# Optimization experiments

Measured on AMD Instinct MI355X. Metric: run time of the kernel, lower is better.

Reference implementation:

```python
import jax, jax.numpy as jnp
import numpy as np

T, B, S = 50, 64, 100
H, C = 512, 512
V_TGT, V_EXT = 32000, 5000
UNK = 0  # ext_dict.stoi[UNK_WORD]


def setup_inputs() -> dict:
    key = jax.random.key(0)
    ks = jax.random.split(key, 8)
    return {
        "hidden": jax.random.normal(ks[0], (T, B, H), jnp.float32),
        "dec_rnn_output": jax.random.normal(ks[1], (T, B, H), jnp.float32),
        "concat_c": jax.random.normal(ks[2], (T, B, H + C), jnp.float32),
        "attn": jax.random.uniform(ks[3], (T, B, S), jnp.float32),
        "copy_to_ext": jax.random.randint(ks[4], (S, B), 0, V_EXT, jnp.int64),
        "W": jax.random.normal(ks[5], (V_TGT, H), jnp.float32) * 0.02,
        "b": jnp.zeros((V_TGT,), jnp.float32),
        "Wc": jax.random.normal(ks[6], (1, H), jnp.float32) * 0.02,
        "bc": jnp.zeros((1,), jnp.float32),
    }


def _safe_log(v):
    return jnp.log(jnp.clip(v, 0.001, 1.0 - 0.001))


def reference(hidden, dec_rnn_output, concat_c, attn, copy_to_ext, W, b, Wc, bc):
    # standard softmax over tgt vocab
    logits = jnp.einsum("tbh,vh->tbv", hidden, W) + b          # [T,B,V_TGT]
    prob_log = jax.nn.log_softmax(logits, axis=-1)
    # copy gate p(z) from decoder hidden (copy_prb == 'hidden')
    copy = jax.nn.sigmoid(jnp.einsum("tbh,oh->tbo", dec_rnn_output, Wc) + bc)  # [T,B,1]
    mul_attn = attn * (1.0 - copy)                              # [T,B,S]
    # onehot+bmm == masked scatter-add of attn mass into ext-vocab bins
    mask = (copy_to_ext != UNK).astype(mul_attn.dtype)          # [S,B]
    aw = mul_attn * mask.T[None]                                # [T,B,S]

    def scatter_one(a_ts, idx_s):  # a_ts [T,S], idx_s [S]
        return jnp.zeros((T, V_EXT), a_ts.dtype).at[:, idx_s].add(a_ts)

    ext_copy_prob = jax.vmap(scatter_one, in_axes=(1, 1), out_axes=1)(aw, copy_to_ext)  # [T,B,V_EXT]
    ext_copy_prob_log = _safe_log(ext_copy_prob)
    return jnp.concatenate([prob_log, ext_copy_prob_log], axis=-1)  # [T,B,V_TGT+V_EXT]
```

## Files before the change

### kernel.cpp

```cpp
#include <hip/hip_runtime.h>
#include <hip/hip_bf16.h>

#define TT 50
#define BB 64
#define SS 100
#define HH 512
#define VT 32000
#define VE 5000
#define LDC 37000
#define MROWS 3200
#define NTILE 250
#define TSTR 136

typedef __bf16 bf16x8 __attribute__((ext_vector_type(8)));
typedef float f32x4 __attribute__((ext_vector_type(4)));

__device__ __forceinline__ ushort f2bf(float f) {
    unsigned u = __float_as_uint(f);
    u += 0x7fffu + ((u >> 16) & 1u);
    return (ushort)(u >> 16);
}
__device__ __forceinline__ float bflo(unsigned u) { return __uint_as_float(u << 16); }
__device__ __forceinline__ float bfhi(unsigned u) { return __uint_as_float(u & 0xffff0000u); }

__global__ void convert_kernel(const float* __restrict__ W, const float* __restrict__ hid,
                               ushort* __restrict__ wsB, ushort* __restrict__ wsA) {
    int g = blockIdx.x * 256 + threadIdx.x;
    const int WG = 4096000;
    float4 v;
    ushort* dst;
    if (g < WG) {
        v = ((const float4*)W)[g];
        dst = wsB + 4 * (size_t)g;
    } else {
        int h = g - WG;
        v = ((const float4*)hid)[h];
        dst = wsA + 4 * (size_t)h;
    }
    ushort4 o;
    o.x = f2bf(v.x); o.y = f2bf(v.y); o.z = f2bf(v.z); o.w = f2bf(v.w);
    *(ushort4*)dst = o;
}

__global__ __launch_bounds__(256) void gemm_kernel(const ushort* __restrict__ A,
                                                   const ushort* __restrict__ B,
                                                   const float* __restrict__ bias,
                                                   ushort* __restrict__ outu,
                                                   float* __restrict__ pm,
                                                   float* __restrict__ ps) {
    __shared__ char smem[34816];
    const int tid  = threadIdx.x;
    const int w    = tid >> 6;
    const int lane = tid & 63;
    const int wr   = w >> 1, wc = w & 1;
    const int brow = blockIdx.y * 128;
    const int bcol = blockIdx.x * 128;
    const int lr   = lane & 15;
    const int kg   = lane >> 4;

    ushort* tileT = (ushort*)smem;
    const int c0 = tid, c1 = tid + 256;
    const int r0 = c0 >> 2, k0 = c0 & 3;
    const int r1 = c1 >> 2, k1 = c1 & 3;

    f32x4 acc[4][4];
#pragma unroll
    for (int m = 0; m < 4; ++m)
#pragma unroll
        for (int n = 0; n < 4; ++n)
            acc[m][n] = (f32x4){0.f, 0.f, 0.f, 0.f};

#define STAGE(buf, kt)                                                                      \
    do {                                                                                    \
        char* bA = smem + (buf) * 8192;                                                     \
        char* bB = smem + 16384 + (buf) * 8192;                                             \
        __builtin_amdgcn_global_load_lds(                                                   \
            (const __attribute__((address_space(1))) void*)(A + (size_t)(brow + r0) * HH + (kt) * 32 + k0 * 8), \
            (__attribute__((address_space(3))) void*)(bA + c0 * 16), 16, 0, 0);             \
        __builtin_amdgcn_global_load_lds(                                                   \
            (const __attribute__((address_space(1))) void*)(A + (size_t)(brow + r1) * HH + (kt) * 32 + k1 * 8), \
            (__attribute__((address_space(3))) void*)(bA + c1 * 16), 16, 0, 0);             \
        __builtin_amdgcn_global_load_lds(                                                   \
            (const __attribute__((address_space(1))) void*)(B + (size_t)(bcol + r0) * HH + (kt) * 32 + k0 * 8), \
            (__attribute__((address_space(3))) void*)(bB + c0 * 16), 16, 0, 0);             \
        __builtin_amdgcn_global_load_lds(                                                   \
            (const __attribute__((address_space(1))) void*)(B + (size_t)(bcol + r1) * HH + (kt) * 32 + k1 * 8), \
            (__attribute__((address_space(3))) void*)(bB + c1 * 16), 16, 0, 0);             \
    } while (0)

    STAGE(0, 0);
    for (int kt = 0; kt < 16; ++kt) {
        const int cur = kt & 1;
        if (kt < 15) {
            STAGE(cur ^ 1, kt + 1);
            asm volatile("s_waitcnt vmcnt(4)" ::: "memory");
        } else {
            asm volatile("s_waitcnt vmcnt(0)" ::: "memory");
        }
        __builtin_amdgcn_sched_barrier(0);
        __builtin_amdgcn_s_barrier();
        __builtin_amdgcn_sched_barrier(0);

        const char* pa = smem + cur * 8192;
        const char* pb = smem + 16384 + cur * 8192;
        bf16x8 af[4], bfr[4];
#pragma unroll
        for (int m = 0; m < 4; ++m)
            af[m] = *(const bf16x8*)(pa + (wr * 64 + m * 16 + lr) * 64 + kg * 16);
#pragma unroll
        for (int n = 0; n < 4; ++n)
            bfr[n] = *(const bf16x8*)(pb + (wc * 64 + n * 16 + lr) * 64 + kg * 16);
#pragma unroll
        for (int m = 0; m < 4; ++m)
#pragma unroll
            for (int n = 0; n < 4; ++n)
                acc[m][n] = __builtin_amdgcn_mfma_f32_16x16x32_bf16(af[m], bfr[n], acc[m][n], 0, 0, 0);

        __builtin_amdgcn_sched_barrier(0);
        __builtin_amdgcn_s_barrier();
    }
#undef STAGE
    __syncthreads();

#pragma unroll
    for (int n = 0; n < 4; ++n) {
        int col = wc * 64 + n * 16 + lr;
        float bv = bias[bcol + col];
#pragma unroll
        for (int m = 0; m < 4; ++m) {
            int row0 = wr * 64 + m * 16 + kg * 4;
#pragma unroll
            for (int r = 0; r < 4; ++r)
                tileT[(row0 + r) * TSTR + col] = f2bf(acc[m][n][r] + bv);
        }
    }
    __syncthreads();

#pragma unroll
    for (int it = 0; it < 8; ++it) {
        int idx = it * 256 + tid;
        int row = idx >> 4, ch = idx & 15;
        uint4 v = *(const uint4*)(&tileT[row * TSTR + ch * 8]);
        *(uint4*)(outu + (size_t)(brow + row) * 74000 + 42000 + bcol + ch * 8) = v;
    }

    {
        int prow = tid >> 1, half = tid & 1;
        const ushort* trow = &tileT[prow * TSTR + half * 64];
        uint4 vv[8];
#pragma unroll
        for (int i = 0; i < 8; ++i) vv[i] = *(const uint4*)(trow + i * 8);
        float mx = -1e30f;
#pragma unroll
        for (int i = 0; i < 8; ++i) {
            mx = fmaxf(mx, fmaxf(fmaxf(bflo(vv[i].x), bfhi(vv[i].x)), fmaxf(bflo(vv[i].y), bfhi(vv[i].y))));
            mx = fmaxf(mx, fmaxf(fmaxf(bflo(vv[i].z), bfhi(vv[i].z)), fmaxf(bflo(vv[i].w), bfhi(vv[i].w))));
        }
        float sx = 0.f;
#pragma unroll
        for (int i = 0; i < 8; ++i) {
            sx += __expf(bflo(vv[i].x) - mx) + __expf(bfhi(vv[i].x) - mx)
                + __expf(bflo(vv[i].y) - mx) + __expf(bfhi(vv[i].y) - mx)
                + __expf(bflo(vv[i].z) - mx) + __expf(bfhi(vv[i].z) - mx)
                + __expf(bflo(vv[i].w) - mx) + __expf(bfhi(vv[i].w) - mx);
        }
        float om = __shfl_xor(mx, 1), os = __shfl_xor(sx, 1);
        float M = fmaxf(mx, om);
        float S = sx * __expf(mx - M) + os * __expf(om - M);
        if (half == 0) {
            pm[(size_t)blockIdx.x * MROWS + brow + prow] = M;
            ps[(size_t)blockIdx.x * MROWS + brow + prow] = S;
        }
    }
}

__global__ __launch_bounds__(256) void norm_ext_kernel(float* __restrict__ out,
                                                       const float* __restrict__ pm,
                                                       const float* __restrict__ ps,
                                                       const float* __restrict__ dec,
                                                       const float* __restrict__ wc,
                                                       const float* __restrict__ bcp,
                                                       const float* __restrict__ attn,
                                                       const int* __restrict__ cte) {
    const int r = blockIdx.x;
    const int t = threadIdx.x;
    const int w = t >> 6, lane = t & 63;
    __shared__ float sm[4], ssv[4], red[4];
    __shared__ float lse_sh, csh;
    __shared__ float bins[VE];

    float m = -1e30f, s = 0.f;
    if (t < NTILE) {
        m = pm[(size_t)t * MROWS + r];
        s = ps[(size_t)t * MROWS + r];
    }
    for (int off = 1; off < 64; off <<= 1) {
        float om = __shfl_xor(m, off), os = __shfl_xor(s, off);
        float nm = fmaxf(m, om);
        s = s * __expf(m - nm) + os * __expf(om - nm);
        m = nm;
    }
    if (lane == 0) { sm[w] = m; ssv[w] = s; }

    {
        float part = dec[(size_t)r * HH + t] * wc[t]
                   + dec[(size_t)r * HH + t + 256] * wc[t + 256];
        for (int off = 1; off < 64; off <<= 1) part += __shfl_xor(part, off);
        if (lane == 0) red[w] = part;
    }
    for (int v = t; v < VE; v += 256) bins[v] = 0.f;
    __syncthreads();

    if (t == 0) {
        float M = sm[0], S = ssv[0];
        for (int i = 1; i < 4; ++i) {
            float nm = fmaxf(M, sm[i]);
            S = S * __expf(M - nm) + ssv[i] * __expf(sm[i] - nm);
            M = nm;
        }
        lse_sh = M + __logf(S);
        float g = red[0] + red[1] + red[2] + red[3] + bcp[0];
        csh = 1.f / (1.f + __expf(-g));
    }
    __syncthreads();
    const float l = lse_sh;
    const float c = csh;

    if (t < SS) {
        float aw = attn[(size_t)r * SS + t] * (1.f - c);
        int idx = cte[t * BB + (r & 63)];
        if (idx != 0) atomicAdd(&bins[idx], aw);
    }

    const uint4* gsrc = (const uint4*)((const ushort*)out + (size_t)r * 74000 + 42000);
    float4* orow = (float4*)(out + (size_t)r * LDC);
    for (int n = 0; n < 16; ++n) {
        int i = t + 256 * n;
        if (i < VT / 8) {
            uint4 v = gsrc[i];
            float4 a, b;
            a.x = bflo(v.x) - l; a.y = bfhi(v.x) - l;
            a.z = bflo(v.y) - l; a.w = bfhi(v.y) - l;
            b.x = bflo(v.z) - l; b.y = bfhi(v.z) - l;
            b.z = bflo(v.w) - l; b.w = bfhi(v.w) - l;
            orow[2 * i]     = a;
            orow[2 * i + 1] = b;
        }
        if ((n & 1) == 1) __syncthreads();
    }
    __syncthreads();

    float4* eo = (float4*)(out + (size_t)r * LDC + VT);
    for (int v = t; v < VE / 4; v += 256) {
        float4 x;
        x.x = __logf(fminf(fmaxf(bins[4 * v + 0], 0.001f), 0.999f));
        x.y = __logf(fminf(fmaxf(bins[4 * v + 1], 0.001f), 0.999f));
        x.z = __logf(fminf(fmaxf(bins[4 * v + 2], 0.001f), 0.999f));
        x.w = __logf(fminf(fmaxf(bins[4 * v + 3], 0.001f), 0.999f));
        eo[v] = x;
    }
}

extern "C" void kernel_launch(void* const* d_in, const int* in_sizes, int n_in,
                              void* d_out, int out_size, void* d_ws, size_t ws_size,
                              hipStream_t stream) {
    const float* hidden = (const float*)d_in[0];
    const float* dec    = (const float*)d_in[1];
    const float* attn   = (const float*)d_in[3];
    const int*   cte    = (const int*)d_in[4];
    const float* W      = (const float*)d_in[5];
    const float* bias   = (const float*)d_in[6];
    const float* Wc     = (const float*)d_in[7];
    const float* bc     = (const float*)d_in[8];
    float* out = (float*)d_out;

    ushort* wsB = (ushort*)d_ws;
    ushort* wsA = wsB + (size_t)VT * HH;
    float*  pm  = (float*)(wsA + (size_t)MROWS * HH);
    float*  ps  = pm + (size_t)NTILE * MROWS;

    convert_kernel<<<17600, 256, 0, stream>>>(W, hidden, wsB, wsA);
    gemm_kernel<<<dim3(NTILE, 25), 256, 0, stream>>>(wsA, wsB, bias, (ushort*)out, pm, ps);
    norm_ext_kernel<<<MROWS, 256, 0, stream>>>(out, pm, ps, dec, Wc, bc, attn, cte);
}
```

Before: 349.6 us.

## Widen GEMM block tile to 128x256 with two-pass epilogue

Widens each GEMM block's N tile from 128 to 256 columns, so each wave computes a 64x128 sub-tile with 32 accumulators. The A tile is now reused across twice as many columns, halving redundant A loads and the number of blocks and partial softmax stats (NTILE 125). The epilogue stages the two 128-column halves through shared memory in turn and merges the online max/sum across halves. This doubles accumulator registers, which may lower occupancy, and adds an extra barrier-separated epilogue pass.

```diff
diff --git a/kernel.cpp b/kernel.cpp
--- a/kernel.cpp
+++ b/kernel.cpp
@@ -9,7 +9,7 @@
 #define VE 5000
 #define LDC 37000
 #define MROWS 3200
-#define NTILE 250
+#define NTILE 125
 #define TSTR 136
 
 typedef __bf16 bf16x8 __attribute__((ext_vector_type(8)));
@@ -48,44 +48,46 @@
                                                    ushort* __restrict__ outu,
                                                    float* __restrict__ pm,
                                                    float* __restrict__ ps) {
-    __shared__ char smem[34816];
+    __shared__ char smem[49152];
     const int tid  = threadIdx.x;
     const int w    = tid >> 6;
     const int lane = tid & 63;
     const int wr   = w >> 1, wc = w & 1;
     const int brow = blockIdx.y * 128;
-    const int bcol = blockIdx.x * 128;
+    const int bcol = blockIdx.x * 256;
     const int lr   = lane & 15;
     const int kg   = lane >> 4;
 
     ushort* tileT = (ushort*)smem;
-    const int c0 = tid, c1 = tid + 256;
-    const int r0 = c0 >> 2, k0 = c0 & 3;
-    const int r1 = c1 >> 2, k1 = c1 & 3;
-
-    f32x4 acc[4][4];
+    const int a0 = tid, a1 = tid + 256;
+    const int ar0 = a0 >> 2, ak0 = a0 & 3;
+    const int ar1 = a1 >> 2, ak1 = a1 & 3;
+
+    f32x4 acc[4][8];
 #pragma unroll
     for (int m = 0; m < 4; ++m)
 #pragma unroll
-        for (int n = 0; n < 4; ++n)
+        for (int n = 0; n < 8; ++n)
             acc[m][n] = (f32x4){0.f, 0.f, 0.f, 0.f};
 
 #define STAGE(buf, kt)                                                                      \
     do {                                                                                    \
         char* bA = smem + (buf) * 8192;                                                     \
-        char* bB = smem + 16384 + (buf) * 8192;                                             \
+        char* bB = smem + 16384 + (buf) * 16384;                                            \
         __builtin_amdgcn_global_load_lds(                                                   \
-            (const __attribute__((address_space(1))) void*)(A + (size_t)(brow + r0) * HH + (kt) * 32 + k0 * 8), \
-            (__attribute__((address_space(3))) void*)(bA + c0 * 16), 16, 0, 0);             \
+            (const __attribute__((address_space(1))) void*)(A + (size_t)(brow + ar0) * HH + (kt) * 32 + ak0 * 8), \
+            (__attribute__((address_space(3))) void*)(bA + a0 * 16), 16, 0, 0);             \
         __builtin_amdgcn_global_load_lds(                                                   \
-            (const __attribute__((address_space(1))) void*)(A + (size_t)(brow + r1) * HH + (kt) * 32 + k1 * 8), \
-            (__attribute__((address_space(3))) void*)(bA + c1 * 16), 16, 0, 0);             \
-        __builtin_amdgcn_global_load_lds(                                                   \
-            (const __attribute__((address_space(1))) void*)(B + (size_t)(bcol + r0) * HH + (kt) * 32 + k0 * 8), \
-            (__attribute__((address_space(3))) void*)(bB + c0 * 16), 16, 0, 0);             \
-        __builtin_amdgcn_global_load_lds(                                                   \
-            (const __attribute__((address_space(1))) void*)(B + (size_t)(bcol + r1) * HH + (kt) * 32 + k1 * 8), \
-            (__attribute__((address_space(3))) void*)(bB + c1 * 16), 16, 0, 0);             \
+            (const __attribute__((address_space(1))) void*)(A + (size_t)(brow + ar1) * HH + (kt) * 32 + ak1 * 8), \
+            (__attribute__((address_space(3))) void*)(bA + a1 * 16), 16, 0, 0);             \
+        _Pragma("unroll")                                                                   \
+        for (int j = 0; j < 4; ++j) {                                                       \
+            int c = tid + j * 256;                                                          \
+            int row = c >> 2, kc = c & 3;                                                   \
+            __builtin_amdgcn_global_load_lds(                                               \
+                (const __attribute__((address_space(1))) void*)(B + (size_t)(bcol + row) * HH + (kt) * 32 + kc * 8), \
+                (__attribute__((address_space(3))) void*)(bB + c * 16), 16, 0, 0);          \
+        }                                                                                   \
     } while (0)
 
     STAGE(0, 0);
@@ -93,7 +95,7 @@
         const int cur = kt & 1;
         if (kt < 15) {
             STAGE(cur ^ 1, kt + 1);
-            asm volatile("s_waitcnt vmcnt(4)" ::: "memory");
+            asm volatile("s_waitcnt vmcnt(6)" ::: "memory");
         } else {
             asm volatile("s_waitcnt vmcnt(0)" ::: "memory");
         }
@@ -102,18 +104,18 @@
         __builtin_amdgcn_sched_barrier(0);
 
         const char* pa = smem + cur * 8192;
-        const char* pb = smem + 16384 + cur * 8192;
-        bf16x8 af[4], bfr[4];
+        const char* pb = smem + 16384 + cur * 16384;
+        bf16x8 af[4], bfr[8];
 #pragma unroll
         for (int m = 0; m < 4; ++m)
             af[m] = *(const bf16x8*)(pa + (wr * 64 + m * 16 + lr) * 64 + kg * 16);
 #pragma unroll
-        for (int n = 0; n < 4; ++n)
-            bfr[n] = *(const bf16x8*)(pb + (wc * 64 + n * 16 + lr) * 64 + kg * 16);
+        for (int n = 0; n < 8; ++n)
+            bfr[n] = *(const bf16x8*)(pb + (wc * 128 + n * 16 + lr) * 64 + kg * 16);
 #pragma unroll
         for (int m = 0; m < 4; ++m)
 #pragma unroll
-            for (int n = 0; n < 4; ++n)
+            for (int n = 0; n < 8; ++n)
                 acc[m][n] = __builtin_amdgcn_mfma_f32_16x16x32_bf16(af[m], bfr[n], acc[m][n], 0, 0, 0);
 
         __builtin_amdgcn_sched_barrier(0);
@@ -122,52 +124,65 @@
 #undef STAGE
     __syncthreads();
 
-#pragma unroll
-    for (int n = 0; n < 4; ++n) {
-        int col = wc * 64 + n * 16 + lr;
-        float bv = bias[bcol + col];
-#pragma unroll
-        for (int m = 0; m < 4; ++m) {
-            int row0 = wr * 64 + m * 16 + kg * 4;
-#pragma unroll
-            for (int r = 0; r < 4; ++r)
-                tileT[(row0 + r) * TSTR + col] = f2bf(acc[m][n][r] + bv);
-        }
-    }
-    __syncthreads();
-
-#pragma unroll
-    for (int it = 0; it < 8; ++it) {
-        int idx = it * 256 + tid;
-        int row = idx >> 4, ch = idx & 15;
-        uint4 v = *(const uint4*)(&tileT[row * TSTR + ch * 8]);
-        *(uint4*)(outu + (size_t)(brow + row) * 74000 + 42000 + bcol + ch * 8) = v;
+    const int prow = tid >> 1, phalf = tid & 1;
+    float Mx = -1e30f, Sx = 0.f;
+#pragma unroll
+    for (int h = 0; h < 2; ++h) {
+        if (wc == h) {
+#pragma unroll
+            for (int n = 0; n < 8; ++n) {
+                int col = n * 16 + lr;
+                float bv = bias[bcol + h * 128 + col];
+#pragma unroll
+                for (int m = 0; m < 4; ++m) {
+                    int row0 = wr * 64 + m * 16 + kg * 4;
+#pragma unroll
+                    for (int r = 0; r < 4; ++r)
+                        tileT[(row0 + r) * TSTR + col] = f2bf(acc[m][n][r] + bv);
+                }
+            }
+        }
+        __syncthreads();
+
+#pragma unroll
+        for (int it = 0; it < 8; ++it) {
+            int idx = it * 256 + tid;
+            int row = idx >> 4, ch = idx & 15;
+            uint4 v = *(const uint4*)(&tileT[row * TSTR + ch * 8]);
+            *(uint4*)(outu + (size_t)(brow + row) * 74000 + 42000 + bcol + h * 128 + ch * 8) = v;
+        }
+
+        {
+            const ushort* trow = &tileT[prow * TSTR + phalf * 64];
+            uint4 vv[8];
+#pragma unroll
+            for (int i = 0; i < 8; ++i) vv[i] = *(const uint4*)(trow + i * 8);
+            float mx = -1e30f;
+#pragma unroll
+            for (int i = 0; i < 8; ++i) {
+                mx = fmaxf(mx, fmaxf(fmaxf(bflo(vv[i].x), bfhi(vv[i].x)), fmaxf(bflo(vv[i].y), bfhi(vv[i].y))));
+                mx = fmaxf(mx, fmaxf(fmaxf(bflo(vv[i].z), bfhi(vv[i].z)), fmaxf(bflo(vv[i].w), bfhi(vv[i].w))));
+            }
+            float sx = 0.f;
+#pragma unroll
+            for (int i = 0; i < 8; ++i) {
+                sx += __expf(bflo(vv[i].x) - mx) + __expf(bfhi(vv[i].x) - mx)
+                    + __expf(bflo(vv[i].y) - mx) + __expf(bfhi(vv[i].y) - mx)
+                    + __expf(bflo(vv[i].z) - mx) + __expf(bfhi(vv[i].z) - mx)
+                    + __expf(bflo(vv[i].w) - mx) + __expf(bfhi(vv[i].w) - mx);
+            }
+            float nm = fmaxf(Mx, mx);
+            Sx = Sx * __expf(Mx - nm) + sx * __expf(mx - nm);
+            Mx = nm;
+        }
+        __syncthreads();
     }
 
     {
-        int prow = tid >> 1, half = tid & 1;
-        const ushort* trow = &tileT[prow * TSTR + half * 64];
-        uint4 vv[8];
-#pragma unroll
-        for (int i = 0; i < 8; ++i) vv[i] = *(const uint4*)(trow + i * 8);
-        float mx = -1e30f;
-#pragma unroll
-        for (int i = 0; i < 8; ++i) {
-            mx = fmaxf(mx, fmaxf(fmaxf(bflo(vv[i].x), bfhi(vv[i].x)), fmaxf(bflo(vv[i].y), bfhi(vv[i].y))));
-            mx = fmaxf(mx, fmaxf(fmaxf(bflo(vv[i].z), bfhi(vv[i].z)), fmaxf(bflo(vv[i].w), bfhi(vv[i].w))));
-        }
-        float sx = 0.f;
-#pragma unroll
-        for (int i = 0; i < 8; ++i) {
-            sx += __expf(bflo(vv[i].x) - mx) + __expf(bfhi(vv[i].x) - mx)
-                + __expf(bflo(vv[i].y) - mx) + __expf(bfhi(vv[i].y) - mx)
-                + __expf(bflo(vv[i].z) - mx) + __expf(bfhi(vv[i].z) - mx)
-                + __expf(bflo(vv[i].w) - mx) + __expf(bfhi(vv[i].w) - mx);
-        }
-        float om = __shfl_xor(mx, 1), os = __shfl_xor(sx, 1);
-        float M = fmaxf(mx, om);
-        float S = sx * __expf(mx - M) + os * __expf(om - M);
-        if (half == 0) {
+        float om = __shfl_xor(Mx, 1), os = __shfl_xor(Sx, 1);
+        float M = fmaxf(Mx, om);
+        float S = Sx * __expf(Mx - M) + os * __expf(om - M);
+        if (phalf == 0) {
             pm[(size_t)blockIdx.x * MROWS + brow + prow] = M;
             ps[(size_t)blockIdx.x * MROWS + brow + prow] = S;
         }
```

Measured after the change: 462.1 us. 32.2% more time.

## Enlarge GEMM tiles to 256x256 with triple-buffered LDS, swizzle, and XCD remap

Applied to the files above, without the earlier changes.

Rewrites the logits GEMM to use 256x256 output tiles with 512 threads, a three-slot LDS pipeline that staggers A and B loads, an XOR swizzle of the LDS layout to reduce bank conflicts, s_setprio around the MFMA blocks, and a blockIdx remap that groups neighbouring tiles on the same XCD. The M dimension is padded to 3328 rows, with zero-filled rows written by the convert kernel, and the partial-softmax stats are now computed per 256-column tile in two 128-row halves. The aim is more data reuse per loaded byte and better overlap of loads with compute. In exchange it uses much more LDS and registers per block and adds padded work.

```diff
diff --git a/kernel.cpp b/kernel.cpp
--- a/kernel.cpp
+++ b/kernel.cpp
@@ -9,8 +9,11 @@
 #define VE 5000
 #define LDC 37000
 #define MROWS 3200
-#define NTILE 250
-#define TSTR 136
+#define MPAD 3328
+#define NTILE 125
+#define NRT 13
+#define NWG 1625
+#define TSTR 264
 
 typedef __bf16 bf16x8 __attribute__((ext_vector_type(8)));
 typedef float f32x4 __attribute__((ext_vector_type(4)));
@@ -27,150 +30,208 @@
                                ushort* __restrict__ wsB, ushort* __restrict__ wsA) {
     int g = blockIdx.x * 256 + threadIdx.x;
     const int WG = 4096000;
-    float4 v;
-    ushort* dst;
-    if (g < WG) {
-        v = ((const float4*)W)[g];
-        dst = wsB + 4 * (size_t)g;
+    const int HG = 409600;
+    if (g < WG + HG) {
+        float4 v;
+        ushort* dst;
+        if (g < WG) {
+            v = ((const float4*)W)[g];
+            dst = wsB + 4 * (size_t)g;
+        } else {
+            int h = g - WG;
+            v = ((const float4*)hid)[h];
+            dst = wsA + 4 * (size_t)h;
+        }
+        ushort4 o;
+        o.x = f2bf(v.x); o.y = f2bf(v.y); o.z = f2bf(v.z); o.w = f2bf(v.w);
+        *(ushort4*)dst = o;
     } else {
-        int h = g - WG;
-        v = ((const float4*)hid)[h];
-        dst = wsA + 4 * (size_t)h;
-    }
-    ushort4 o;
-    o.x = f2bf(v.x); o.y = f2bf(v.y); o.z = f2bf(v.z); o.w = f2bf(v.w);
-    *(ushort4*)dst = o;
-}
-
-__global__ __launch_bounds__(256) void gemm_kernel(const ushort* __restrict__ A,
-                                                   const ushort* __restrict__ B,
-                                                   const float* __restrict__ bias,
-                                                   ushort* __restrict__ outu,
-                                                   float* __restrict__ pm,
-                                                   float* __restrict__ ps) {
-    __shared__ char smem[34816];
+        int p = g - (WG + HG);
+        ushort4 z = {0, 0, 0, 0};
+        *(ushort4*)(wsA + (size_t)HG * 4 + 4 * (size_t)p) = z;
+    }
+}
+
+__global__ __launch_bounds__(512, 2) void gemm_kernel(const ushort* __restrict__ A,
+                                                      const ushort* __restrict__ B,
+                                                      const float* __restrict__ bias,
+                                                      ushort* __restrict__ outu,
+                                                      float* __restrict__ pm,
+                                                      float* __restrict__ ps) {
+    __shared__ char smem[98304];
     const int tid  = threadIdx.x;
-    const int w    = tid >> 6;
+    const int wid  = tid >> 6;
     const int lane = tid & 63;
-    const int wr   = w >> 1, wc = w & 1;
-    const int brow = blockIdx.y * 128;
-    const int bcol = blockIdx.x * 128;
+    const int wrow = wid >> 2, wcol = wid & 3;
     const int lr   = lane & 15;
     const int kg   = lane >> 4;
-
-    ushort* tileT = (ushort*)smem;
-    const int c0 = tid, c1 = tid + 256;
-    const int r0 = c0 >> 2, k0 = c0 & 3;
-    const int r1 = c1 >> 2, k1 = c1 & 3;
-
-    f32x4 acc[4][4];
-#pragma unroll
-    for (int m = 0; m < 4; ++m)
+    const int kgs  = kg ^ ((lr >> 1) & 3);
+
+    const int orig = blockIdx.x;
+    const int xcd  = orig & 7, seq = orig >> 3;
+    const int wgid = (xcd == 0 ? 0 : 204 + (xcd - 1) * 203) + seq;
+    const int ct   = wgid / NRT;
+    const int rt   = wgid - ct * NRT;
+    const int brow = rt * 256;
+    const int bcol = ct * 256;
+
+    const int c0 = tid, c1 = tid + 512;
+    const int r0 = c0 >> 2, s0 = (c0 & 3) ^ ((r0 >> 1) & 3);
+    const int r1 = c1 >> 2, s1 = (c1 & 3) ^ ((r1 >> 1) & 3);
+
+    f32x4 acc[8][4];
+#pragma unroll
+    for (int m = 0; m < 8; ++m)
 #pragma unroll
         for (int n = 0; n < 4; ++n)
             acc[m][n] = (f32x4){0.f, 0.f, 0.f, 0.f};
 
-#define STAGE(buf, kt)                                                                      \
+#define LDSA(s) (smem + (s) * 16384)
+#define LDSB(s) (smem + 49152 + (s) * 16384)
+#define STAGE_A(slot, kt)                                                                   \
     do {                                                                                    \
-        char* bA = smem + (buf) * 8192;                                                     \
-        char* bB = smem + 16384 + (buf) * 8192;                                             \
         __builtin_amdgcn_global_load_lds(                                                   \
-            (const __attribute__((address_space(1))) void*)(A + (size_t)(brow + r0) * HH + (kt) * 32 + k0 * 8), \
-            (__attribute__((address_space(3))) void*)(bA + c0 * 16), 16, 0, 0);             \
+            (const __attribute__((address_space(1))) void*)(A + (size_t)(brow + r0) * HH + (kt) * 32 + s0 * 8), \
+            (__attribute__((address_space(3))) void*)(LDSA(slot) + c0 * 16), 16, 0, 0);     \
         __builtin_amdgcn_global_load_lds(                                                   \
-            (const __attribute__((address_space(1))) void*)(A + (size_t)(brow + r1) * HH + (kt) * 32 + k1 * 8), \
-            (__attribute__((address_space(3))) void*)(bA + c1 * 16), 16, 0, 0);             \
+            (const __attribute__((address_space(1))) void*)(A + (size_t)(brow + r1) * HH + (kt) * 32 + s1 * 8), \
+            (__attribute__((address_space(3))) void*)(LDSA(slot) + c1 * 16), 16, 0, 0);     \
+    } while (0)
+#define STAGE_B(slot, kt)                                                                   \
+    do {                                                                                    \
         __builtin_amdgcn_global_load_lds(                                                   \
-            (const __attribute__((address_space(1))) void*)(B + (size_t)(bcol + r0) * HH + (kt) * 32 + k0 * 8), \
-            (__attribute__((address_space(3))) void*)(bB + c0 * 16), 16, 0, 0);             \
+            (const __attribute__((address_space(1))) void*)(B + (size_t)(bcol + r0) * HH + (kt) * 32 + s0 * 8), \
+            (__attribute__((address_space(3))) void*)(LDSB(slot) + c0 * 16), 16, 0, 0);     \
         __builtin_amdgcn_global_load_lds(                                                   \
-            (const __attribute__((address_space(1))) void*)(B + (size_t)(bcol + r1) * HH + (kt) * 32 + k1 * 8), \
-            (__attribute__((address_space(3))) void*)(bB + c1 * 16), 16, 0, 0);             \
+            (const __attribute__((address_space(1))) void*)(B + (size_t)(bcol + r1) * HH + (kt) * 32 + s1 * 8), \
+            (__attribute__((address_space(3))) void*)(LDSB(slot) + c1 * 16), 16, 0, 0);     \
     } while (0)
 
-    STAGE(0, 0);
-    for (int kt = 0; kt < 16; ++kt) {
-        const int cur = kt & 1;
-        if (kt < 15) {
-            STAGE(cur ^ 1, kt + 1);
+    STAGE_A(0, 0); STAGE_B(0, 0); STAGE_A(1, 1); STAGE_B(1, 1);
+
+    int slot = 0;
+    for (int t = 0; t < 16; ++t) {
+        const int sl2 = (slot + 2 >= 3) ? slot - 1 : slot + 2;
+        const char* pa = (const char*)LDSA(slot);
+        const char* pb = (const char*)LDSB(slot);
+        bf16x8 af[4], bf[4];
+
+        if (t < 14) {
+            STAGE_A(sl2, t + 2);
+            asm volatile("s_waitcnt vmcnt(6)" ::: "memory");
+        } else if (t == 14) {
             asm volatile("s_waitcnt vmcnt(4)" ::: "memory");
         } else {
             asm volatile("s_waitcnt vmcnt(0)" ::: "memory");
         }
+        __builtin_amdgcn_s_barrier();
+        asm volatile("" ::: "memory");
+#pragma unroll
+        for (int n = 0; n < 4; ++n)
+            bf[n] = *(const bf16x8*)(pb + ((wcol * 64 + n * 16 + lr) * 64 + kgs * 16));
+#pragma unroll
+        for (int m = 0; m < 4; ++m)
+            af[m] = *(const bf16x8*)(pa + ((wrow * 128 + m * 16 + lr) * 64 + kgs * 16));
         __builtin_amdgcn_sched_barrier(0);
+        __builtin_amdgcn_s_setprio(1);
+#pragma unroll
+        for (int m = 0; m < 4; ++m)
+#pragma unroll
+            for (int n = 0; n < 4; ++n)
+                acc[m][n] = __builtin_amdgcn_mfma_f32_16x16x32_bf16(af[m], bf[n], acc[m][n], 0, 0, 0);
+        __builtin_amdgcn_s_setprio(0);
+        asm volatile("" ::: "memory");
         __builtin_amdgcn_s_barrier();
+        asm volatile("" ::: "memory");
+
+        if (t < 14) STAGE_B(sl2, t + 2);
+#pragma unroll
+        for (int m = 0; m < 4; ++m)
+            af[m] = *(const bf16x8*)(pa + ((wrow * 128 + 64 + m * 16 + lr) * 64 + kgs * 16));
         __builtin_amdgcn_sched_barrier(0);
-
-        const char* pa = smem + cur * 8192;
-        const char* pb = smem + 16384 + cur * 8192;
-        bf16x8 af[4], bfr[4];
+        __builtin_amdgcn_s_setprio(1);
 #pragma unroll
         for (int m = 0; m < 4; ++m)
-            af[m] = *(const bf16x8*)(pa + (wr * 64 + m * 16 + lr) * 64 + kg * 16);
-#pragma unroll
-        for (int n = 0; n < 4; ++n)
-            bfr[n] = *(const bf16x8*)(pb + (wc * 64 + n * 16 + lr) * 64 + kg * 16);
-#pragma unroll
-        for (int m = 0; m < 4; ++m)
 #pragma unroll
             for (int n = 0; n < 4; ++n)
-                acc[m][n] = __builtin_amdgcn_mfma_f32_16x16x32_bf16(af[m], bfr[n], acc[m][n], 0, 0, 0);
-
-        __builtin_amdgcn_sched_barrier(0);
+                acc[4 + m][n] = __builtin_amdgcn_mfma_f32_16x16x32_bf16(af[m], bf[n], acc[4 + m][n], 0, 0, 0);
+        __builtin_amdgcn_s_setprio(0);
+        asm volatile("" ::: "memory");
         __builtin_amdgcn_s_barrier();
-    }
-#undef STAGE
+        asm volatile("" ::: "memory");
+
+        slot = (slot == 2) ? 0 : slot + 1;
+    }
+#undef STAGE_A
+#undef STAGE_B
+#undef LDSA
+#undef LDSB
     __syncthreads();
 
-#pragma unroll
-    for (int n = 0; n < 4; ++n) {
-        int col = wc * 64 + n * 16 + lr;
-        float bv = bias[bcol + col];
-#pragma unroll
-        for (int m = 0; m < 4; ++m) {
-            int row0 = wr * 64 + m * 16 + kg * 4;
-#pragma unroll
-            for (int r = 0; r < 4; ++r)
-                tileT[(row0 + r) * TSTR + col] = f2bf(acc[m][n][r] + bv);
-        }
-    }
-    __syncthreads();
-
-#pragma unroll
-    for (int it = 0; it < 8; ++it) {
-        int idx = it * 256 + tid;
-        int row = idx >> 4, ch = idx & 15;
-        uint4 v = *(const uint4*)(&tileT[row * TSTR + ch * 8]);
-        *(uint4*)(outu + (size_t)(brow + row) * 74000 + 42000 + bcol + ch * 8) = v;
-    }
-
-    {
-        int prow = tid >> 1, half = tid & 1;
-        const ushort* trow = &tileT[prow * TSTR + half * 64];
-        uint4 vv[8];
-#pragma unroll
-        for (int i = 0; i < 8; ++i) vv[i] = *(const uint4*)(trow + i * 8);
-        float mx = -1e30f;
-#pragma unroll
-        for (int i = 0; i < 8; ++i) {
-            mx = fmaxf(mx, fmaxf(fmaxf(bflo(vv[i].x), bfhi(vv[i].x)), fmaxf(bflo(vv[i].y), bfhi(vv[i].y))));
-            mx = fmaxf(mx, fmaxf(fmaxf(bflo(vv[i].z), bfhi(vv[i].z)), fmaxf(bflo(vv[i].w), bfhi(vv[i].w))));
-        }
-        float sx = 0.f;
-#pragma unroll
-        for (int i = 0; i < 8; ++i) {
-            sx += __expf(bflo(vv[i].x) - mx) + __expf(bfhi(vv[i].x) - mx)
-                + __expf(bflo(vv[i].y) - mx) + __expf(bfhi(vv[i].y) - mx)
-                + __expf(bflo(vv[i].z) - mx) + __expf(bfhi(vv[i].z) - mx)
-                + __expf(bflo(vv[i].w) - mx) + __expf(bfhi(vv[i].w) - mx);
-        }
-        float om = __shfl_xor(mx, 1), os = __shfl_xor(sx, 1);
-        float M = fmaxf(mx, om);
-        float S = sx * __expf(mx - M) + os * __expf(om - M);
-        if (half == 0) {
-            pm[(size_t)blockIdx.x * MROWS + brow + prow] = M;
-            ps[(size_t)blockIdx.x * MROWS + brow + prow] = S;
-        }
+    ushort* tileT = (ushort*)smem;
+    const int prow = tid >> 2, pq = tid & 3;
+#pragma unroll
+    for (int h = 0; h < 2; ++h) {
+        if (wrow == h) {
+#pragma unroll
+            for (int n = 0; n < 4; ++n) {
+                int col = wcol * 64 + n * 16 + lr;
+                float bv = bias[bcol + col];
+#pragma unroll
+                for (int m = 0; m < 8; ++m) {
+                    int row0 = m * 16 + kg * 4;
+#pragma unroll
+                    for (int r = 0; r < 4; ++r)
+                        tileT[(row0 + r) * TSTR + col] = f2bf(acc[m][n][r] + bv);
+                }
+            }
+        }
+        __syncthreads();
+
+#pragma unroll
+        for (int it = 0; it < 8; ++it) {
+            int idx = it * 512 + tid;
+            int row = idx >> 5, ch = idx & 31;
+            int grow = brow + h * 128 + row;
+            if (grow < MROWS) {
+                uint4 v = *(const uint4*)(&tileT[row * TSTR + ch * 8]);
+                *(uint4*)(outu + (size_t)grow * 74000 + 42000 + bcol + ch * 8) = v;
+            }
+        }
+
+        {
+            int grow = brow + h * 128 + prow;
+            const ushort* trow = &tileT[prow * TSTR + pq * 64];
+            uint4 vv[8];
+#pragma unroll
+            for (int i = 0; i < 8; ++i) vv[i] = *(const uint4*)(trow + i * 8);
+            float mx = -1e30f;
+#pragma unroll
+            for (int i = 0; i < 8; ++i) {
+                mx = fmaxf(mx, fmaxf(fmaxf(bflo(vv[i].x), bfhi(vv[i].x)), fmaxf(bflo(vv[i].y), bfhi(vv[i].y))));
+                mx = fmaxf(mx, fmaxf(fmaxf(bflo(vv[i].z), bfhi(vv[i].z)), fmaxf(bflo(vv[i].w), bfhi(vv[i].w))));
+            }
+            float sx = 0.f;
+#pragma unroll
+            for (int i = 0; i < 8; ++i) {
+                sx += __expf(bflo(vv[i].x) - mx) + __expf(bfhi(vv[i].x) - mx)
+                    + __expf(bflo(vv[i].y) - mx) + __expf(bfhi(vv[i].y) - mx)
+                    + __expf(bflo(vv[i].z) - mx) + __expf(bfhi(vv[i].z) - mx)
+                    + __expf(bflo(vv[i].w) - mx) + __expf(bfhi(vv[i].w) - mx);
+            }
+#pragma unroll
+            for (int off = 1; off < 4; off <<= 1) {
+                float om = __shfl_xor(mx, off), os = __shfl_xor(sx, off);
+                float nm = fmaxf(mx, om);
+                sx = sx * __expf(mx - nm) + os * __expf(om - nm);
+                mx = nm;
+            }
+            if (pq == 0 && grow < MROWS) {
+                pm[(size_t)ct * MROWS + grow] = mx;
+                ps[(size_t)ct * MROWS + grow] = sx;
+            }
+        }
+        __syncthreads();
     }
 }
 
@@ -276,10 +337,10 @@
 
     ushort* wsB = (ushort*)d_ws;
     ushort* wsA = wsB + (size_t)VT * HH;
-    float*  pm  = (float*)(wsA + (size_t)MROWS * HH);
+    float*  pm  = (float*)(wsA + (size_t)MPAD * HH);
     float*  ps  = pm + (size_t)NTILE * MROWS;
 
-    convert_kernel<<<17600, 256, 0, stream>>>(W, hidden, wsB, wsA);
-    gemm_kernel<<<dim3(NTILE, 25), 256, 0, stream>>>(wsA, wsB, bias, (ushort*)out, pm, ps);
+    convert_kernel<<<17664, 256, 0, stream>>>(W, hidden, wsB, wsA);
+    gemm_kernel<<<NWG, 512, 0, stream>>>(wsA, wsB, bias, (ushort*)out, pm, ps);
     norm_ext_kernel<<<MROWS, 256, 0, stream>>>(out, pm, ps, dec, Wc, bc, attn, cte);
 }
```

After: 354.4 us. About the same (+1.4%).
